# Performance work log

Measured on AMD Instinct MI355X. Metric: run time of the kernel, lower is better.

## Reference

```python
import jax, jax.numpy as jnp
import numpy as np

LAYER_SIZES = [4096, 8192, 8192, 4096, 1024]
BATCH = 4096
SCARCITY = 0.05


def setup_inputs() -> dict:
    key = jax.random.key(0)
    ks = jax.random.split(key, 5)
    inp = {"x": jax.random.normal(ks[0], (LAYER_SIZES[0], BATCH), dtype=jnp.float32)}
    for i in range(4):
        out_d, in_d = LAYER_SIZES[i + 1], LAYER_SIZES[i]
        # uniform(-0.1, 0.1) mirrors the repo's weight_initialization(a=-0.1, b=0.1)
        inp[f"W{i}"] = jax.random.uniform(ks[i + 1], (out_d, in_d), dtype=jnp.float32,
                                          minval=-0.1, maxval=0.1)
        inp[f"thr{i}"] = jnp.ones((out_d,), dtype=jnp.float32)  # starting_threshold = 1.0
    return inp


def _kwta(x, thr, k):
    # x: [out, batch]; per-column k-winners-take-all on (x - thr)
    act = x - thr[:, None]
    kth = jax.lax.top_k(act.T, k)[0][:, -1]          # [batch] k-th largest per column
    mask = act >= kth[None, :]
    return jnp.where(mask, x, jnp.zeros_like(x))


def reference(x, W0, W1, W2, W3, thr0, thr1, thr2, thr3):
    Ws = [W0, W1, W2, W3]
    thrs = [thr0, thr1, thr2, thr3]
    n_layers = len(Ws)
    for i in range(n_layers):
        x = Ws[i] @ x                                 # [out_i, batch]
        if i < n_layers - 1:
            x = jax.nn.relu(x)
        k = int(SCARCITY * Ws[i].shape[0])
        x = _kwta(x, thrs[i], k)
    return jax.nn.softmax(x, axis=0)                  # output_activation over features
```

## Files before the change

### kernel.cpp

```cpp
#include <hip/hip_runtime.h>

typedef _Float16 f16x8 __attribute__((ext_vector_type(8)));
typedef _Float16 f16x4 __attribute__((ext_vector_type(4)));
typedef float f32x4 __attribute__((ext_vector_type(4)));

#define NB 4096

__device__ __forceinline__ void gload16(const void* g, void* l) {
    __builtin_amdgcn_global_load_lds(
        (const __attribute__((address_space(1))) unsigned int*)g,
        (__attribute__((address_space(3))) unsigned int*)l, 16, 0, 0);
}

__global__ __launch_bounds__(256) void tsplit_kernel(const float* __restrict__ X,
                                                     _Float16* __restrict__ Oh,
                                                     _Float16* __restrict__ Ol) {
    __shared__ float t[64][65];
    const int f0 = blockIdx.x * 64, b0 = blockIdx.y * 64;
    const int tid = threadIdx.x;
    const int jj = tid & 63, i0 = tid >> 6;
#pragma unroll
    for (int p = 0; p < 16; ++p) {
        int i = p * 4 + i0;
        t[i][jj] = X[(size_t)(f0 + i) * NB + b0 + jj];
    }
    __syncthreads();
#pragma unroll
    for (int p = 0; p < 16; ++p) {
        int b = p * 4 + i0;
        float v = t[jj][b];
        size_t idx = (size_t)(b0 + b) * 4096 + f0 + jj;
        _Float16 h = (_Float16)v;
        Oh[idx] = h;
        Ol[idx] = (_Float16)((v - (float)h) * 2048.0f);
    }
}

__global__ __launch_bounds__(256) void splitw_kernel(const float* __restrict__ W,
                                                     _Float16* __restrict__ Wh,
                                                     _Float16* __restrict__ Wl, long n4) {
    long i = (long)blockIdx.x * 256 + threadIdx.x;
    const long stride = (long)gridDim.x * 256;
    for (; i < n4; i += stride) {
        float4 w = ((const float4*)W)[i];
        float vs[4] = {w.x, w.y, w.z, w.w};
        f16x4 h, l;
#pragma unroll
        for (int j = 0; j < 4; ++j) {
            _Float16 hh = (_Float16)vs[j];
            h[j] = hh;
            l[j] = (_Float16)((vs[j] - (float)hh) * 2048.0f);
        }
        ((f16x4*)Wh)[i] = h;
        ((f16x4*)Wl)[i] = l;
    }
}

__global__ __launch_bounds__(256, 2) void gemm3_kernel(
    const _Float16* __restrict__ Ah, const _Float16* __restrict__ Al,
    const _Float16* __restrict__ Bh, const _Float16* __restrict__ Bl,
    float* __restrict__ C, int K, int M, int do_relu) {
    __shared__ __align__(16) _Float16 sAh[128 * 32];
    __shared__ __align__(16) _Float16 sAl[128 * 32];
    __shared__ __align__(16) _Float16 sBh[128 * 32];
    __shared__ __align__(16) _Float16 sBl[128 * 32];

    const int tid = threadIdx.x;
    const int row0 = blockIdx.y * 128;
    const int col0 = blockIdx.x * 128;
    const int wid = tid >> 6, lane = tid & 63;
    const int wm = wid >> 1, wn = wid & 1;
    const int lr = lane & 15, lk = (lane >> 4) * 8;

    f32x4 acc[4][4] = {};
    f32x4 accx[4][4] = {};

    const int o0 = tid * 16;
    const int o1 = o0 + 4096;
    const int r0 = o0 >> 6, c0 = o0 & 63;
    const int r1 = o1 >> 6, c1 = o1 & 63;
    const size_t sk = (size_t)K * 2;

    const char* gAh0 = (const char*)Ah + (size_t)(row0 + r0) * sk + c0;
    const char* gAh1 = (const char*)Ah + (size_t)(row0 + r1) * sk + c1;
    const char* gAl0 = (const char*)Al + (size_t)(row0 + r0) * sk + c0;
    const char* gAl1 = (const char*)Al + (size_t)(row0 + r1) * sk + c1;
    const char* gBh0 = (const char*)Bh + (size_t)(col0 + r0) * sk + c0;
    const char* gBh1 = (const char*)Bh + (size_t)(col0 + r1) * sk + c1;
    const char* gBl0 = (const char*)Bl + (size_t)(col0 + r0) * sk + c0;
    const char* gBl1 = (const char*)Bl + (size_t)(col0 + r1) * sk + c1;

    for (int k0 = 0; k0 < K; k0 += 32) {
        __syncthreads();
        gload16(gAh0, (char*)sAh + o0);
        gload16(gAh1, (char*)sAh + o1);
        gload16(gAl0, (char*)sAl + o0);
        gload16(gAl1, (char*)sAl + o1);
        gload16(gBh0, (char*)sBh + o0);
        gload16(gBh1, (char*)sBh + o1);
        gload16(gBl0, (char*)sBl + o0);
        gload16(gBl1, (char*)sBl + o1);
        gAh0 += 64; gAh1 += 64; gAl0 += 64; gAl1 += 64;
        gBh0 += 64; gBh1 += 64; gBl0 += 64; gBl1 += 64;
        __syncthreads();

        f16x8 bh[4], bl[4];
#pragma unroll
        for (int ni = 0; ni < 4; ++ni) {
            int rb = wn * 64 + ni * 16 + lr;
            bh[ni] = *(const f16x8*)&sBh[rb * 32 + lk];
            bl[ni] = *(const f16x8*)&sBl[rb * 32 + lk];
        }
#pragma unroll
        for (int mi = 0; mi < 4; ++mi) {
            int ra = wm * 64 + mi * 16 + lr;
            f16x8 ah = *(const f16x8*)&sAh[ra * 32 + lk];
            f16x8 al = *(const f16x8*)&sAl[ra * 32 + lk];
#pragma unroll
            for (int ni = 0; ni < 4; ++ni) {
                acc[mi][ni] = __builtin_amdgcn_mfma_f32_16x16x32_f16(ah, bh[ni], acc[mi][ni], 0, 0, 0);
                accx[mi][ni] = __builtin_amdgcn_mfma_f32_16x16x32_f16(ah, bl[ni], accx[mi][ni], 0, 0, 0);
                accx[mi][ni] = __builtin_amdgcn_mfma_f32_16x16x32_f16(al, bh[ni], accx[mi][ni], 0, 0, 0);
            }
        }
    }
#pragma unroll
    for (int mi = 0; mi < 4; ++mi)
#pragma unroll
        for (int ni = 0; ni < 4; ++ni) {
            int colx = col0 + wn * 64 + ni * 16 + lr;
            int rowb = row0 + wm * 64 + mi * 16 + (lane >> 4) * 4;
#pragma unroll
            for (int r = 0; r < 4; ++r) {
                float v = acc[mi][ni][r] + accx[mi][ni][r] * (1.0f / 2048.0f);
                if (do_relu) v = fmaxf(v, 0.0f);
                C[(size_t)(rowb + r) * M + colx] = v;
            }
        }
}

template <int CNT, bool SOFTMAX>
__global__ __launch_bounds__(256) void kwta_kernel(const float* __restrict__ Cin,
                                                   const float* __restrict__ thr,
                                                   _Float16* __restrict__ Oh,
                                                   _Float16* __restrict__ Ol,
                                                   float* __restrict__ outT, int M, int k) {
    const int row = blockIdx.x, tid = threadIdx.x;
    const float* rp = Cin + (size_t)row * M;
    unsigned uv[CNT];
    float xv[CNT];
#pragma unroll
    for (int i = 0; i < CNT; ++i) {
        int col = i * 256 + tid;
        float x = rp[col];
        float a = x - thr[col];
        unsigned b = __float_as_uint(a);
        uv[i] = (b & 0x80000000u) ? ~b : (b | 0x80000000u);
        xv[i] = x;
    }
    __shared__ int hist[256];
    __shared__ unsigned sel_s;
    __shared__ int kk_s;
    unsigned prefix = 0;
    int kk = k;
#pragma unroll
    for (int pass = 0; pass < 4; ++pass) {
        const int shift = 24 - pass * 8;
        hist[tid] = 0;
        __syncthreads();
#pragma unroll
        for (int i = 0; i < CNT; ++i) {
            bool ok = (pass == 0) || ((uv[i] >> (shift + 8)) == prefix);
            if (ok) atomicAdd(&hist[(uv[i] >> shift) & 255], 1);
        }
        __syncthreads();
        for (int off = 1; off < 256; off <<= 1) {
            int v = hist[tid] + ((tid + off < 256) ? hist[tid + off] : 0);
            __syncthreads();
            hist[tid] = v;
            __syncthreads();
        }
        if (hist[tid] >= kk && (tid == 255 || hist[tid + 1] < kk)) {
            sel_s = (unsigned)tid;
            kk_s = kk - ((tid == 255) ? 0 : hist[tid + 1]);
        }
        __syncthreads();
        prefix = (prefix << 8) | sel_s;
        kk = kk_s;
        __syncthreads();
    }
    const unsigned kth = prefix;
    if (!SOFTMAX) {
#pragma unroll
        for (int i = 0; i < CNT; ++i) {
            int col = i * 256 + tid;
            float v = (uv[i] >= kth) ? xv[i] : 0.0f;
            size_t idx = (size_t)row * M + col;
            _Float16 h = (_Float16)v;
            Oh[idx] = h;
            Ol[idx] = (_Float16)((v - (float)h) * 2048.0f);
        }
    } else {
        float vals[CNT];
        float m = -3.4e38f;
#pragma unroll
        for (int i = 0; i < CNT; ++i) {
            float v = (uv[i] >= kth) ? xv[i] : 0.0f;
            vals[i] = v;
            m = fmaxf(m, v);
        }
        for (int off = 32; off; off >>= 1) m = fmaxf(m, __shfl_xor(m, off));
        __shared__ float redm[4];
        if ((tid & 63) == 0) redm[tid >> 6] = m;
        __syncthreads();
        m = fmaxf(fmaxf(redm[0], redm[1]), fmaxf(redm[2], redm[3]));
        float s = 0.0f, e[CNT];
#pragma unroll
        for (int i = 0; i < CNT; ++i) {
            e[i] = expf(vals[i] - m);
            s += e[i];
        }
        for (int off = 32; off; off >>= 1) s += __shfl_xor(s, off);
        __shared__ float reds[4];
        if ((tid & 63) == 0) reds[tid >> 6] = s;
        __syncthreads();
        s = reds[0] + reds[1] + reds[2] + reds[3];
        float inv = 1.0f / s;
#pragma unroll
        for (int i = 0; i < CNT; ++i)
            outT[(size_t)(i * 256 + tid) * NB + row] = e[i] * inv;
    }
}

extern "C" void kernel_launch(void* const* d_in, const int* in_sizes, int n_in,
                              void* d_out, int out_size, void* d_ws, size_t ws_size,
                              hipStream_t stream) {
    const float* x = (const float*)d_in[0];
    const float* W0 = (const float*)d_in[1];
    const float* thr0 = (const float*)d_in[2];
    const float* W1 = (const float*)d_in[3];
    const float* thr1 = (const float*)d_in[4];
    const float* W2 = (const float*)d_in[5];
    const float* thr2 = (const float*)d_in[6];
    const float* W3 = (const float*)d_in[7];
    const float* thr3 = (const float*)d_in[8];
    float* out = (float*)d_out;

    char* ws = (char*)d_ws;
    size_t off = 0;
    auto alloc = [&](size_t bytes) {
        void* p = ws + off;
        off += (bytes + 255) & ~(size_t)255;
        return p;
    };
    _Float16* Wh = (_Float16*)alloc((size_t)8192 * 8192 * 2);
    _Float16* Wl = (_Float16*)alloc((size_t)8192 * 8192 * 2);
    _Float16* Xh = (_Float16*)alloc((size_t)4096 * 8192 * 2);
    _Float16* Xl = (_Float16*)alloc((size_t)4096 * 8192 * 2);
    _Float16* Yh = (_Float16*)alloc((size_t)4096 * 8192 * 2);
    _Float16* Yl = (_Float16*)alloc((size_t)4096 * 8192 * 2);
    float* C32 = (float*)alloc((size_t)4096 * 8192 * 4);

    tsplit_kernel<<<dim3(64, 64), 256, 0, stream>>>(x, Xh, Xl);

    splitw_kernel<<<4096, 256, 0, stream>>>(W0, Wh, Wl, (long)8192 * 4096 / 4);
    gemm3_kernel<<<dim3(8192 / 128, NB / 128), 256, 0, stream>>>(Xh, Xl, Wh, Wl, C32, 4096, 8192, 1);
    kwta_kernel<32, false><<<NB, 256, 0, stream>>>(C32, thr0, Yh, Yl, nullptr, 8192, 409);

    splitw_kernel<<<4096, 256, 0, stream>>>(W1, Wh, Wl, (long)8192 * 8192 / 4);
    gemm3_kernel<<<dim3(8192 / 128, NB / 128), 256, 0, stream>>>(Yh, Yl, Wh, Wl, C32, 8192, 8192, 1);
    kwta_kernel<32, false><<<NB, 256, 0, stream>>>(C32, thr1, Xh, Xl, nullptr, 8192, 409);

    splitw_kernel<<<4096, 256, 0, stream>>>(W2, Wh, Wl, (long)4096 * 8192 / 4);
    gemm3_kernel<<<dim3(4096 / 128, NB / 128), 256, 0, stream>>>(Xh, Xl, Wh, Wl, C32, 8192, 4096, 1);
    kwta_kernel<16, false><<<NB, 256, 0, stream>>>(C32, thr2, Yh, Yl, nullptr, 4096, 204);

    splitw_kernel<<<4096, 256, 0, stream>>>(W3, Wh, Wl, (long)1024 * 4096 / 4);
    gemm3_kernel<<<dim3(1024 / 128, NB / 128), 256, 0, stream>>>(Yh, Yl, Wh, Wl, C32, 4096, 1024, 0);
    kwta_kernel<4, true><<<NB, 256, 0, stream>>>(C32, thr3, nullptr, nullptr, out, 1024, 51);
}
```

Measured before the change: 3.809 ms.

## Add 512-thread 128x256 triple-buffered split-fp16 GEMM for first three layers

```diff
diff --git a/kernel.cpp b/kernel.cpp
--- a/kernel.cpp
+++ b/kernel.cpp
@@ -54,6 +54,124 @@
         ((f16x4*)Wh)[i] = h;
         ((f16x4*)Wl)[i] = l;
     }
+}
+
+__global__ __launch_bounds__(512, 2) void gemm3p_kernel(
+    const _Float16* __restrict__ Ah, const _Float16* __restrict__ Al,
+    const _Float16* __restrict__ Bh, const _Float16* __restrict__ Bl,
+    float* __restrict__ C, int K, int M, int do_relu) {
+    __shared__ __align__(16) char lds[3][49152];
+
+    const int tid = threadIdx.x;
+    const int gx = gridDim.x;
+    const int nwg = gx * gridDim.y;
+    int bid = blockIdx.y * gx + blockIdx.x;
+    bid = (bid & 7) * (nwg >> 3) + (bid >> 3);
+    const int col0 = (bid % gx) * 256;
+    const int row0 = (bid / gx) * 128;
+
+    const int wid = tid >> 6, lane = tid & 63;
+    const int wm = wid >> 2, wn = wid & 3;
+    const int lr = lane & 15;
+    const int rdoff = (((lane >> 4) ^ ((lane >> 1) & 3)) << 4);
+
+    f32x4 acc[4][4] = {};
+    f32x4 accx[4][4] = {};
+
+    const int srow = tid >> 2;
+    const int scl = (tid & 3) ^ ((tid >> 3) & 3);
+    const size_t sk = (size_t)K;
+    const _Float16* gA_h = Ah + (size_t)(row0 + srow) * sk + scl * 8;
+    const _Float16* gA_l = Al + (size_t)(row0 + srow) * sk + scl * 8;
+    const _Float16* gB_h0 = Bh + (size_t)(col0 + srow) * sk + scl * 8;
+    const _Float16* gB_h1 = Bh + (size_t)(col0 + 128 + srow) * sk + scl * 8;
+    const _Float16* gB_l0 = Bl + (size_t)(col0 + srow) * sk + scl * 8;
+    const _Float16* gB_l1 = Bl + (size_t)(col0 + 128 + srow) * sk + scl * 8;
+    const int ldsA = tid * 16;
+
+#define STAGE(bufi, t2)                                   \
+    do {                                                  \
+        char* Lb = lds[bufi];                             \
+        const size_t go = (size_t)(t2) * 32;              \
+        gload16(gA_h + go, Lb + ldsA);                    \
+        gload16(gA_l + go, Lb + 8192 + ldsA);             \
+        gload16(gB_h0 + go, Lb + 16384 + ldsA);           \
+        gload16(gB_h1 + go, Lb + 24576 + ldsA);           \
+        gload16(gB_l0 + go, Lb + 32768 + ldsA);           \
+        gload16(gB_l1 + go, Lb + 40960 + ldsA);           \
+    } while (0)
+
+    const int NT = K / 32;
+    STAGE(0, 0);
+    STAGE(1, 1);
+
+    for (int t = 0; t < NT; ++t) {
+        if (t < NT - 1) {
+            asm volatile("s_waitcnt vmcnt(6)" ::: "memory");
+        } else {
+            asm volatile("s_waitcnt vmcnt(0)" ::: "memory");
+        }
+        __builtin_amdgcn_s_barrier();
+        asm volatile("" ::: "memory");
+        if (t + 2 < NT) STAGE((t + 2) % 3, t + 2);
+
+        const char* Lb = lds[t % 3];
+        const char* sAh_ = Lb;
+        const char* sAl_ = Lb + 8192;
+        const char* sBh_ = Lb + 16384;
+        const char* sBl_ = Lb + 32768;
+
+        f16x8 ah[4], al[4], bh[4], bl[4];
+#pragma unroll
+        for (int mi = 0; mi < 4; ++mi) {
+            const int ra = wm * 64 + mi * 16 + lr;
+            ah[mi] = *(const f16x8*)(sAh_ + ra * 64 + rdoff);
+            al[mi] = *(const f16x8*)(sAl_ + ra * 64 + rdoff);
+        }
+#pragma unroll
+        for (int ni = 0; ni < 2; ++ni) {
+            const int rb = wn * 64 + ni * 16 + lr;
+            bh[ni] = *(const f16x8*)(sBh_ + rb * 64 + rdoff);
+            bl[ni] = *(const f16x8*)(sBl_ + rb * 64 + rdoff);
+        }
+#pragma unroll
+        for (int ni = 0; ni < 4; ++ni) {
+            if (ni < 3) {
+                asm volatile("s_waitcnt lgkmcnt(2)" ::: "memory");
+            } else {
+                asm volatile("s_waitcnt lgkmcnt(0)" ::: "memory");
+            }
+            if (ni < 2) {
+                const int rb = wn * 64 + (ni + 2) * 16 + lr;
+                bh[ni + 2] = *(const f16x8*)(sBh_ + rb * 64 + rdoff);
+                bl[ni + 2] = *(const f16x8*)(sBl_ + rb * 64 + rdoff);
+            }
+            __builtin_amdgcn_sched_barrier(0);
+            __builtin_amdgcn_s_setprio(1);
+#pragma unroll
+            for (int mi = 0; mi < 4; ++mi) {
+                acc[mi][ni] = __builtin_amdgcn_mfma_f32_16x16x32_f16(ah[mi], bh[ni], acc[mi][ni], 0, 0, 0);
+                accx[mi][ni] = __builtin_amdgcn_mfma_f32_16x16x32_f16(ah[mi], bl[ni], accx[mi][ni], 0, 0, 0);
+                accx[mi][ni] = __builtin_amdgcn_mfma_f32_16x16x32_f16(al[mi], bh[ni], accx[mi][ni], 0, 0, 0);
+            }
+            __builtin_amdgcn_s_setprio(0);
+        }
+    }
+#undef STAGE
+
+#pragma unroll
+    for (int mi = 0; mi < 4; ++mi)
+#pragma unroll
+        for (int ni = 0; ni < 4; ++ni) {
+            int colx = col0 + wn * 64 + ni * 16 + lr;
+            int rowb = row0 + wm * 64 + mi * 16 + ((lane >> 4) << 2);
+#pragma unroll
+            for (int r = 0; r < 4; ++r) {
+                float v = acc[mi][ni][r] + accx[mi][ni][r] * (1.0f / 2048.0f);
+                if (do_relu) v = fmaxf(v, 0.0f);
+                C[(size_t)(rowb + r) * M + colx] = v;
+            }
+        }
 }
 
 __global__ __launch_bounds__(256, 2) void gemm3_kernel(
@@ -264,15 +382,15 @@
     tsplit_kernel<<<dim3(64, 64), 256, 0, stream>>>(x, Xh, Xl);
 
     splitw_kernel<<<4096, 256, 0, stream>>>(W0, Wh, Wl, (long)8192 * 4096 / 4);
-    gemm3_kernel<<<dim3(8192 / 128, NB / 128), 256, 0, stream>>>(Xh, Xl, Wh, Wl, C32, 4096, 8192, 1);
+    gemm3p_kernel<<<dim3(8192 / 256, NB / 128), 512, 0, stream>>>(Xh, Xl, Wh, Wl, C32, 4096, 8192, 1);
     kwta_kernel<32, false><<<NB, 256, 0, stream>>>(C32, thr0, Yh, Yl, nullptr, 8192, 409);
 
     splitw_kernel<<<4096, 256, 0, stream>>>(W1, Wh, Wl, (long)8192 * 8192 / 4);
-    gemm3_kernel<<<dim3(8192 / 128, NB / 128), 256, 0, stream>>>(Yh, Yl, Wh, Wl, C32, 8192, 8192, 1);
+    gemm3p_kernel<<<dim3(8192 / 256, NB / 128), 512, 0, stream>>>(Yh, Yl, Wh, Wl, C32, 8192, 8192, 1);
     kwta_kernel<32, false><<<NB, 256, 0, stream>>>(C32, thr1, Xh, Xl, nullptr, 8192, 409);
 
     splitw_kernel<<<4096, 256, 0, stream>>>(W2, Wh, Wl, (long)4096 * 8192 / 4);
-    gemm3_kernel<<<dim3(4096 / 128, NB / 128), 256, 0, stream>>>(Xh, Xl, Wh, Wl, C32, 8192, 4096, 1);
+    gemm3p_kernel<<<dim3(4096 / 256, NB / 128), 512, 0, stream>>>(Xh, Xl, Wh, Wl, C32, 8192, 4096, 1);
     kwta_kernel<16, false><<<NB, 256, 0, stream>>>(C32, thr2, Yh, Yl, nullptr, 4096, 204);
 
     splitw_kernel<<<4096, 256, 0, stream>>>(W3, Wh, Wl, (long)1024 * 4096 / 4);
```

After: 5.242 ms. 37.6% more time.

## Pipeline split-fp16 GEMM with triple-buffered LDS, swizzle, and tile rasterization

Applied to the files above, without the earlier changes.

```diff
diff --git a/kernel.cpp b/kernel.cpp
--- a/kernel.cpp
+++ b/kernel.cpp
@@ -56,80 +56,115 @@
     }
 }
 
-__global__ __launch_bounds__(256, 2) void gemm3_kernel(
+__global__ __launch_bounds__(256, 1) void gemm3p_kernel(
     const _Float16* __restrict__ Ah, const _Float16* __restrict__ Al,
     const _Float16* __restrict__ Bh, const _Float16* __restrict__ Bl,
     float* __restrict__ C, int K, int M, int do_relu) {
-    __shared__ __align__(16) _Float16 sAh[128 * 32];
-    __shared__ __align__(16) _Float16 sAl[128 * 32];
-    __shared__ __align__(16) _Float16 sBh[128 * 32];
-    __shared__ __align__(16) _Float16 sBl[128 * 32];
+    __shared__ __align__(16) char lds[3][32768];
 
     const int tid = threadIdx.x;
-    const int row0 = blockIdx.y * 128;
-    const int col0 = blockIdx.x * 128;
+    const int gx = gridDim.x;
+    int bid = blockIdx.y * gx + blockIdx.x;
+    const int SC = gx < 16 ? gx : 16;
+    const int SR = 256 / SC;
+    const int nsc = gx / SC;
+    const int s = bid >> 8, w = bid & 255;
+    const int col0 = ((s % nsc) * SC + (w % SC)) * 128;
+    const int row0 = ((s / nsc) * SR + (w / SC)) * 128;
+
     const int wid = tid >> 6, lane = tid & 63;
     const int wm = wid >> 1, wn = wid & 1;
-    const int lr = lane & 15, lk = (lane >> 4) * 8;
+    const int lr = lane & 15;
+    const int rdoff = (((lane >> 4) ^ ((lane >> 1) & 3)) << 4);
 
     f32x4 acc[4][4] = {};
     f32x4 accx[4][4] = {};
 
-    const int o0 = tid * 16;
-    const int o1 = o0 + 4096;
-    const int r0 = o0 >> 6, c0 = o0 & 63;
-    const int r1 = o1 >> 6, c1 = o1 & 63;
-    const size_t sk = (size_t)K * 2;
-
-    const char* gAh0 = (const char*)Ah + (size_t)(row0 + r0) * sk + c0;
-    const char* gAh1 = (const char*)Ah + (size_t)(row0 + r1) * sk + c1;
-    const char* gAl0 = (const char*)Al + (size_t)(row0 + r0) * sk + c0;
-    const char* gAl1 = (const char*)Al + (size_t)(row0 + r1) * sk + c1;
-    const char* gBh0 = (const char*)Bh + (size_t)(col0 + r0) * sk + c0;
-    const char* gBh1 = (const char*)Bh + (size_t)(col0 + r1) * sk + c1;
-    const char* gBl0 = (const char*)Bl + (size_t)(col0 + r0) * sk + c0;
-    const char* gBl1 = (const char*)Bl + (size_t)(col0 + r1) * sk + c1;
-
-    for (int k0 = 0; k0 < K; k0 += 32) {
-        __syncthreads();
-        gload16(gAh0, (char*)sAh + o0);
-        gload16(gAh1, (char*)sAh + o1);
-        gload16(gAl0, (char*)sAl + o0);
-        gload16(gAl1, (char*)sAl + o1);
-        gload16(gBh0, (char*)sBh + o0);
-        gload16(gBh1, (char*)sBh + o1);
-        gload16(gBl0, (char*)sBl + o0);
-        gload16(gBl1, (char*)sBl + o1);
-        gAh0 += 64; gAh1 += 64; gAl0 += 64; gAl1 += 64;
-        gBh0 += 64; gBh1 += 64; gBl0 += 64; gBl1 += 64;
-        __syncthreads();
-
-        f16x8 bh[4], bl[4];
-#pragma unroll
-        for (int ni = 0; ni < 4; ++ni) {
-            int rb = wn * 64 + ni * 16 + lr;
-            bh[ni] = *(const f16x8*)&sBh[rb * 32 + lk];
-            bl[ni] = *(const f16x8*)&sBl[rb * 32 + lk];
-        }
-#pragma unroll
-        for (int mi = 0; mi < 4; ++mi) {
-            int ra = wm * 64 + mi * 16 + lr;
-            f16x8 ah = *(const f16x8*)&sAh[ra * 32 + lk];
-            f16x8 al = *(const f16x8*)&sAl[ra * 32 + lk];
-#pragma unroll
-            for (int ni = 0; ni < 4; ++ni) {
-                acc[mi][ni] = __builtin_amdgcn_mfma_f32_16x16x32_f16(ah, bh[ni], acc[mi][ni], 0, 0, 0);
-                accx[mi][ni] = __builtin_amdgcn_mfma_f32_16x16x32_f16(ah, bl[ni], accx[mi][ni], 0, 0, 0);
-                accx[mi][ni] = __builtin_amdgcn_mfma_f32_16x16x32_f16(al, bh[ni], accx[mi][ni], 0, 0, 0);
-            }
-        }
-    }
+    const int srow = tid >> 2;
+    const int scl = (tid & 3) ^ ((tid >> 3) & 3);
+    const size_t sk = (size_t)K;
+    const _Float16* gA_h = Ah + (size_t)(row0 + srow) * sk + scl * 8;
+    const _Float16* gA_h2 = gA_h + 64 * sk;
+    const _Float16* gA_l = Al + (size_t)(row0 + srow) * sk + scl * 8;
+    const _Float16* gA_l2 = gA_l + 64 * sk;
+    const _Float16* gB_h = Bh + (size_t)(col0 + srow) * sk + scl * 8;
+    const _Float16* gB_h2 = gB_h + 64 * sk;
+    const _Float16* gB_l = Bl + (size_t)(col0 + srow) * sk + scl * 8;
+    const _Float16* gB_l2 = gB_l + 64 * sk;
+    const int ldsA = tid * 16;
+
+#define STAGE(Lb, t2)                                         \
+    do {                                                      \
+        const size_t go = (size_t)(t2) * 32;                  \
+        char* L_ = (Lb);                                      \
+        gload16(gA_h + go, L_ + ldsA);                        \
+        gload16(gA_h2 + go, L_ + 4096 + ldsA);                \
+        gload16(gA_l + go, L_ + 8192 + ldsA);                 \
+        gload16(gA_l2 + go, L_ + 12288 + ldsA);               \
+        gload16(gB_h + go, L_ + 16384 + ldsA);                \
+        gload16(gB_h2 + go, L_ + 20480 + ldsA);               \
+        gload16(gB_l + go, L_ + 24576 + ldsA);                \
+        gload16(gB_l2 + go, L_ + 28672 + ldsA);               \
+    } while (0)
+
+#define READF(Lb, ah_, al_, bh_, bl_)                                        \
+    do {                                                                     \
+        const char* L_ = (Lb);                                               \
+        _Pragma("unroll") for (int i = 0; i < 4; ++i) {                      \
+            const int ra = wm * 64 + i * 16 + lr;                            \
+            const int rb = wn * 64 + i * 16 + lr;                            \
+            ah_[i] = *(const f16x8*)(L_ + ra * 64 + rdoff);                  \
+            al_[i] = *(const f16x8*)(L_ + 8192 + ra * 64 + rdoff);           \
+            bh_[i] = *(const f16x8*)(L_ + 16384 + rb * 64 + rdoff);          \
+            bl_[i] = *(const f16x8*)(L_ + 24576 + rb * 64 + rdoff);          \
+        }                                                                    \
+    } while (0)
+
+#define MFMA16(ah_, al_, bh_, bl_)                                                                       \
+    do {                                                                                                 \
+        _Pragma("unroll") for (int mi = 0; mi < 4; ++mi) _Pragma("unroll") for (int ni = 0; ni < 4; ++ni) { \
+            acc[mi][ni] = __builtin_amdgcn_mfma_f32_16x16x32_f16(ah_[mi], bh_[ni], acc[mi][ni], 0, 0, 0);   \
+            accx[mi][ni] = __builtin_amdgcn_mfma_f32_16x16x32_f16(ah_[mi], bl_[ni], accx[mi][ni], 0, 0, 0);  \
+            accx[mi][ni] = __builtin_amdgcn_mfma_f32_16x16x32_f16(al_[mi], bh_[ni], accx[mi][ni], 0, 0, 0);  \
+        }                                                                                                \
+    } while (0)
+
+    f16x8 ahA[4], alA[4], bhA[4], blA[4];
+    f16x8 ahB[4], alB[4], bhB[4], blB[4];
+
+    const int NT = K / 32;
+    STAGE(lds[0], 0);
+    STAGE(lds[1], 1);
+    asm volatile("s_waitcnt vmcnt(8)" ::: "memory");
+    __builtin_amdgcn_s_barrier();
+    READF(lds[0], ahA, alA, bhA, blA);
+
+    for (int t = 0; t < NT; t += 2) {
+        asm volatile("s_waitcnt vmcnt(0)" ::: "memory");
+        __builtin_amdgcn_s_barrier();
+        READF(lds[(t + 1) % 3], ahB, alB, bhB, blB);
+        if (t + 2 < NT) STAGE(lds[(t + 2) % 3], t + 2);
+        __builtin_amdgcn_sched_barrier(0);
+        MFMA16(ahA, alA, bhA, blA);
+        if (t + 2 < NT) {
+            asm volatile("s_waitcnt vmcnt(0)" ::: "memory");
+            __builtin_amdgcn_s_barrier();
+            READF(lds[(t + 2) % 3], ahA, alA, bhA, blA);
+            if (t + 3 < NT) STAGE(lds[(t + 3) % 3], t + 3);
+            __builtin_amdgcn_sched_barrier(0);
+        }
+        MFMA16(ahB, alB, bhB, blB);
+    }
+#undef STAGE
+#undef READF
+#undef MFMA16
+
 #pragma unroll
     for (int mi = 0; mi < 4; ++mi)
 #pragma unroll
         for (int ni = 0; ni < 4; ++ni) {
             int colx = col0 + wn * 64 + ni * 16 + lr;
-            int rowb = row0 + wm * 64 + mi * 16 + (lane >> 4) * 4;
+            int rowb = row0 + wm * 64 + mi * 16 + ((lane >> 4) << 2);
 #pragma unroll
             for (int r = 0; r < 4; ++r) {
                 float v = acc[mi][ni][r] + accx[mi][ni][r] * (1.0f / 2048.0f);
@@ -264,18 +299,18 @@
     tsplit_kernel<<<dim3(64, 64), 256, 0, stream>>>(x, Xh, Xl);
 
     splitw_kernel<<<4096, 256, 0, stream>>>(W0, Wh, Wl, (long)8192 * 4096 / 4);
-    gemm3_kernel<<<dim3(8192 / 128, NB / 128), 256, 0, stream>>>(Xh, Xl, Wh, Wl, C32, 4096, 8192, 1);
+    gemm3p_kernel<<<dim3(8192 / 128, NB / 128), 256, 0, stream>>>(Xh, Xl, Wh, Wl, C32, 4096, 8192, 1);
     kwta_kernel<32, false><<<NB, 256, 0, stream>>>(C32, thr0, Yh, Yl, nullptr, 8192, 409);
 
     splitw_kernel<<<4096, 256, 0, stream>>>(W1, Wh, Wl, (long)8192 * 8192 / 4);
-    gemm3_kernel<<<dim3(8192 / 128, NB / 128), 256, 0, stream>>>(Yh, Yl, Wh, Wl, C32, 8192, 8192, 1);
+    gemm3p_kernel<<<dim3(8192 / 128, NB / 128), 256, 0, stream>>>(Yh, Yl, Wh, Wl, C32, 8192, 8192, 1);
     kwta_kernel<32, false><<<NB, 256, 0, stream>>>(C32, thr1, Xh, Xl, nullptr, 8192, 409);
 
     splitw_kernel<<<4096, 256, 0, stream>>>(W2, Wh, Wl, (long)4096 * 8192 / 4);
-    gemm3_kernel<<<dim3(4096 / 128, NB / 128), 256, 0, stream>>>(Xh, Xl, Wh, Wl, C32, 8192, 4096, 1);
+    gemm3p_kernel<<<dim3(4096 / 128, NB / 128), 256, 0, stream>>>(Xh, Xl, Wh, Wl, C32, 8192, 4096, 1);
     kwta_kernel<16, false><<<NB, 256, 0, stream>>>(C32, thr2, Yh, Yl, nullptr, 4096, 204);
 
     splitw_kernel<<<4096, 256, 0, stream>>>(W3, Wh, Wl, (long)1024 * 4096 / 4);
-    gemm3_kernel<<<dim3(1024 / 128, NB / 128), 256, 0, stream>>>(Yh, Yl, Wh, Wl, C32, 4096, 1024, 0);
+    gemm3p_kernel<<<dim3(1024 / 128, NB / 128), 256, 0, stream>>>(Yh, Yl, Wh, Wl, C32, 4096, 1024, 0);
     kwta_kernel<4, true><<<NB, 256, 0, stream>>>(C32, thr3, nullptr, nullptr, out, 1024, 51);
 }
```

Result: slower. 5.311 ms (+39.4%).
